# Performance work log

Measured on AMD Instinct MI355X. Metric: run time of the kernel, lower is better.

The kernel has to match this reference:

```python
import jax, jax.numpy as jnp
import numpy as np

B, D, H, Z, E = 65536, 128, 256, 128, 16  # batch, input, hidden, hyper, embedding


def setup_inputs() -> dict:
    key = jax.random.key(0)
    ks = jax.random.split(key, 20)
    s = 0.02  # small weight scale for numerical sanity
    return {
        "x": jax.random.normal(ks[0], (B, D), jnp.float32),
        "h0": jax.random.normal(ks[1], (B, H), jnp.float32),
        "c0": jax.random.normal(ks[2], (B, H), jnp.float32),
        "hhat0": jax.random.normal(ks[3], (B, Z), jnp.float32),
        "chat0": jax.random.normal(ks[4], (B, Z), jnp.float32),
        "hweight": jax.random.normal(ks[5], (Z + H + D, 4 * Z), jnp.float32) * s,
        "hbias": jnp.zeros((4 * Z,), jnp.float32),
        "zw_h": jax.random.normal(ks[6], (Z, 4 * E), jnp.float32) * s,
        "zw_x": jax.random.normal(ks[7], (Z, 4 * E), jnp.float32) * s,
        "zw_b": jax.random.normal(ks[8], (Z, 4 * E), jnp.float32) * 0.01,
        "zb_h": jnp.ones((4 * E,), jnp.float32),
        "zb_x": jnp.ones((4 * E,), jnp.float32),
        "dw_h": jnp.full((4, E, H), 0.1 / E, jnp.float32),  # [i,g,f,o] stacked
        "dw_x": jnp.full((4, E, H), 0.1 / E, jnp.float32),
        "dw_b": jax.random.normal(ks[9], (4, E, H), jnp.float32) * s,
        "weight": jax.random.normal(ks[10], (H + D, 4 * H), jnp.float32) * s,
        "bias": jnp.zeros((4 * H,), jnp.float32),
    }


def reference(x, h0, c0, hhat0, chat0, hweight, hbias, zw_h, zw_x, zw_b,
              zb_h, zb_x, dw_h, dw_x, dw_b, weight, bias):
    sig, tanh = jax.nn.sigmoid, jnp.tanh
    b = x.shape[0]
    # hyper LSTM cell
    gh = jnp.concatenate([hhat0, h0, x], axis=1) @ hweight + hbias  # [B, 4Z]
    i_h, g_h, f_h, o_h = jnp.split(gh, 4, axis=1)
    chat1 = sig(f_h) * chat0 + sig(i_h) * tanh(g_h)
    hhat1 = sig(o_h) * tanh(chat1)
    # embedding projections z (chunk order i,g,f,o -> reshape to [B,4,E])
    z_h = (hhat1 @ zw_h + zb_h).reshape(b, 4, E)
    z_x = (hhat1 @ zw_x + zb_x).reshape(b, 4, E)
    z_b = (hhat1 @ zw_b).reshape(b, 4, E)
    # d scaling vectors, [B,4,H] -> [B,4H]
    d_yh = jnp.einsum('bke,keh->bkh', z_h, dw_h).reshape(b, 4 * H)
    d_yx = jnp.einsum('bke,keh->bkh', z_x, dw_x).reshape(b, 4 * H)
    d_yb = jnp.einsum('bke,keh->bkh', z_b, dw_b).reshape(b, 4 * H)
    # main LSTM gates, hyper-modulated
    g = jnp.concatenate([h0, x], axis=1) @ weight * d_yh * d_yx + d_yb + bias
    i_g, g_g, f_g, o_g = jnp.split(g, 4, axis=1)
    c1 = sig(f_g) * c0 + sig(i_g) * tanh(g_g)
    h1 = sig(o_g) * tanh(c1)
    return (h1, c1, hhat1, chat1)
```

## Files before the change

### kernel.cpp

```cpp
#include <hip/hip_runtime.h>


typedef unsigned short u16;
typedef __attribute__((ext_vector_type(8))) short bf16x8;
typedef __attribute__((ext_vector_type(4))) float f32x4;

#define BATCH 65536

__device__ __forceinline__ u16 f2b(float f) {
  unsigned u = __float_as_uint(f);
  u += 0x7fffu + ((u >> 16) & 1u);
  return (u16)(u >> 16);
}
__device__ __forceinline__ unsigned pk2(float a, float b) {
  return (unsigned)f2b(a) | ((unsigned)f2b(b) << 16);
}
__device__ __forceinline__ float upk_lo(unsigned u) { return __uint_as_float(u << 16); }
__device__ __forceinline__ float upk_hi(unsigned u) { return __uint_as_float(u & 0xffff0000u); }
__device__ __forceinline__ float sigf(float x) { return 1.0f / (1.0f + __expf(-x)); }
__device__ __forceinline__ float tanhfast(float x) {
  float xc = fminf(fmaxf(x, -15.f), 15.f);
  float e = __expf(2.f * xc);
  return (e - 1.f) / (e + 1.f);
}
__device__ __forceinline__ int swz(int r, int c) { return r * 64 + (c ^ ((r & 7) << 3)); }

__device__ __forceinline__ void wait0_bar() {
  asm volatile("s_waitcnt vmcnt(0)" ::: "memory");
  __builtin_amdgcn_s_barrier();
  __builtin_amdgcn_sched_barrier(0);
}

__device__ __forceinline__ void gl_lds16(const u16* g, u16* l) {
  __builtin_amdgcn_global_load_lds(
      (const __attribute__((address_space(1))) void*)g,
      (__attribute__((address_space(3))) void*)l, 16, 0, 0);
}
__device__ __forceinline__ void stageA(const u16* base, int ldk, u16* lA, int t) {
  const int r = t >> 3, q = t & 7, wid = t >> 6;
  const int qs = (q ^ (r & 7)) << 3;
  gl_lds16(base + (size_t)r * ldk + qs, lA + wid * 512);
  gl_lds16(base + (size_t)(r + 32) * ldk + qs, lA + 2048 + wid * 512);
}
__device__ __forceinline__ void stageB16(const u16* tile, u16* lB, int t) {
  const int wid = t >> 6;
#pragma unroll
  for (int i = 0; i < 4; ++i)
    gl_lds16(tile + ((size_t)i * 256 + t) * 8, lB + i * 2048 + wid * 512);
}

__global__ __launch_bounds__(256) void hlstm_pre(
    const float* __restrict__ hhat0, const float* __restrict__ h0,
    const float* __restrict__ x, u16* __restrict__ abuf,
    const float* __restrict__ hweight, const float* __restrict__ hbias,
    const float* __restrict__ zw_h, const float* __restrict__ zw_x, const float* __restrict__ zw_b,
    const float* __restrict__ zb_h, const float* __restrict__ zb_x,
    const float* __restrict__ dw_h, const float* __restrict__ dw_x, const float* __restrict__ dw_b,
    const float* __restrict__ weight, const float* __restrict__ bias,
    u16* __restrict__ hw_fr, float* __restrict__ hbias_r,
    u16* __restrict__ w_fr,  float* __restrict__ bias_r,
    u16* __restrict__ whp_fr, u16* __restrict__ wxp_fr, u16* __restrict__ wbp_fr,
    float* __restrict__ bhp_r, float* __restrict__ bxp_r)
{
  if (blockIdx.x < 4096) {
    const size_t stride = (size_t)4096 * 256;
    for (size_t i = (size_t)blockIdx.x * 256 + threadIdx.x;
         i < (size_t)BATCH * 64; i += stride) {
      const size_t b = i >> 6; const int c = (int)(i & 63);
      const float* src;
      if (c < 16)      src = hhat0 + b * 128 + c * 8;
      else if (c < 48) src = h0 + b * 256 + (size_t)(c - 16) * 8;
      else             src = x + b * 128 + (size_t)(c - 48) * 8;
      float4 v0 = ((const float4*)src)[0];
      float4 v1 = ((const float4*)src)[1];
      alignas(16) u16 o[8] = {f2b(v0.x), f2b(v0.y), f2b(v0.z), f2b(v0.w),
                              f2b(v1.x), f2b(v1.y), f2b(v1.z), f2b(v1.w)};
      *(uint4*)(abuf + i * 8) = *(const uint4*)o;
    }
    return;
  }
  const int tid = (blockIdx.x - 4096) * 256 + threadIdx.x;
  const int nt  = 512 * 256;

  for (int i = tid; i < 32 * 8192; i += nt) {
    int tile = i >> 13, r = i & 8191;
    int wn = r >> 12, h = (r >> 11) & 1, g = (r >> 9) & 3;
    int lane = (r >> 3) & 63, j = r & 7;
    int hb = tile >> 4, hh32 = (tile >> 3) & 1, s = tile & 7;
    int k = s * 64 + h * 32 + (lane >> 4) * 8 + j;
    int col = g * 128 + hb * 64 + hh32 * 32 + wn * 16 + (lane & 15);
    hw_fr[i] = f2b(hweight[k * 512 + col]);
  }
  for (int i = tid; i < 48 * 8192; i += nt) {
    int tile = i >> 13, r = i & 8191;
    int wn = r >> 12, h = (r >> 11) & 1, g = (r >> 9) & 3;
    int lane = (r >> 3) & 63, j = r & 7;
    int hb = tile / 12, rem = tile % 12;
    int hh32 = rem / 6, s = rem % 6;
    int k = s * 64 + h * 32 + (lane >> 4) * 8 + j;
    int col = g * 256 + hb * 64 + hh32 * 32 + wn * 16 + (lane & 15);
    w_fr[i] = f2b(weight[k * 1024 + col]);
  }
  for (int i = tid; i < 3 * 16 * 8192; i += nt) {
    int mat = i / 131072, rem2 = i % 131072;
    int tile = rem2 >> 13, r = rem2 & 8191;
    int wn = r >> 12, h = (r >> 11) & 1, g = (r >> 9) & 3;
    int lane = (r >> 3) & 63, j = r & 7;
    int hb = tile >> 2, hh32 = (tile >> 1) & 1, s = tile & 1;
    int k = s * 64 + h * 32 + (lane >> 4) * 8 + j;
    int colh = hb * 64 + hh32 * 32 + wn * 16 + (lane & 15);
    const float* zw = (mat == 0) ? zw_h : (mat == 1) ? zw_x : zw_b;
    const float* dw = (mat == 0) ? dw_h : (mat == 1) ? dw_x : dw_b;
    float sv = 0.f;
#pragma unroll
    for (int e = 0; e < 16; ++e)
      sv += zw[k * 64 + g * 16 + e] * dw[g * 4096 + e * 256 + colh];
    u16* dst = (mat == 0) ? whp_fr : (mat == 1) ? wxp_fr : wbp_fr;
    dst[rem2] = f2b(sv);
  }
  for (int i = tid; i < 1024; i += nt) {
    int hb = i >> 8, g = (i >> 6) & 3, hh = i & 63;
    int h = hb * 64 + hh;
    float sh = 0.f, sx = 0.f;
#pragma unroll
    for (int e = 0; e < 16; ++e) {
      sh += zb_h[g * 16 + e] * dw_h[g * 4096 + e * 256 + h];
      sx += zb_x[g * 16 + e] * dw_x[g * 4096 + e * 256 + h];
    }
    bhp_r[i] = sh; bxp_r[i] = sx;
    bias_r[i] = bias[g * 256 + h];
  }
  for (int i = tid; i < 512; i += nt) {
    int gate = (i >> 6) & 3, hb = i >> 8, hh = i & 63;
    hbias_r[i] = hbias[gate * 128 + hb * 64 + hh];
  }
}

__global__ __launch_bounds__(256, 2) void hlstm_k1(
    const u16* __restrict__ abuf, const float* __restrict__ chat0,
    const u16* __restrict__ hw_fr, const float* __restrict__ hbias_r,
    float* __restrict__ d_out, u16* __restrict__ hbuf)
{
  __shared__ alignas(16) u16 lA[2][8192];
  __shared__ alignas(16) u16 lB[2][8192];
  const int f = blockIdx.x;
  const int xcd = f & 7, u = f >> 3;
  const int rb = xcd * 64 + (u >> 2);
  const int sub = u & 3, hb = sub >> 1, hh32 = sub & 1;
  const int t = threadIdx.x;
  const int lane = t & 63, w = t >> 6;
  const int wm = w >> 1, wn = w & 1;
  const int lr = lane & 15, kg = lane >> 4;

  f32x4 acc[4][4];
  const f32x4 zzero = {0.f, 0.f, 0.f, 0.f};
#pragma unroll
  for (int mf = 0; mf < 4; ++mf)
#pragma unroll
    for (int g = 0; g < 4; ++g) acc[mf][g] = zzero;

  const u16* arow = abuf + (size_t)rb * 128 * 512;
  auto btile = [&](int s) -> const u16* {
    return hw_fr + (size_t)((hb * 2 + hh32) * 8 + s) * 8192;
  };
  auto stage = [&](int s, int buf) {
    stageA(arow + s * 64, 512, lA[buf], t);
    stageA(arow + s * 64 + (size_t)64 * 512, 512, lA[buf] + 4096, t);
    stageB16(btile(s), lB[buf], t);
  };
  auto sweep = [&](const u16* cA, const u16* cB) {
#pragma unroll
    for (int h = 0; h < 2; ++h) {
      bf16x8 bfr[4];
#pragma unroll
      for (int g = 0; g < 4; ++g)
        bfr[g] = *(const bf16x8*)&cB[wn * 4096 + (h * 4 + g) * 512 + lane * 8];
#pragma unroll
      for (int mf = 0; mf < 4; ++mf) {
        bf16x8 afr = *(const bf16x8*)&cA[swz(wm * 64 + mf * 16 + lr, h * 32 + kg * 8)];
#pragma unroll
        for (int g = 0; g < 4; ++g)
          acc[mf][g] = __builtin_amdgcn_mfma_f32_16x16x32_bf16(afr, bfr[g], acc[mf][g], 0, 0, 0);
      }
    }
  };

  stage(0, 0);
  wait0_bar();
#pragma unroll
  for (int ks = 0; ks < 8; ++ks) {
    const int cur = ks & 1;
    if (ks < 7) stage(ks + 1, cur ^ 1);
    sweep(lA[cur], lB[cur]);
    if (ks < 7) wait0_bar();
  }

  float hb4[4];
#pragma unroll
  for (int g = 0; g < 4; ++g)
    hb4[g] = hbias_r[hb * 256 + g * 64 + hh32 * 32 + wn * 16 + lr];
  const int zc = hb * 64 + hh32 * 32 + wn * 16 + lr;
  float* out_hh = d_out + (size_t)BATCH * 512;
  float* out_ch = d_out + (size_t)BATCH * 640;
#pragma unroll
  for (int mf = 0; mf < 4; ++mf)
#pragma unroll
    for (int r = 0; r < 4; ++r) {
      const int row = rb * 128 + wm * 64 + mf * 16 + kg * 4 + r;
      const float gi = acc[mf][0][r] + hb4[0];
      const float gg = acc[mf][1][r] + hb4[1];
      const float gf = acc[mf][2][r] + hb4[2];
      const float go = acc[mf][3][r] + hb4[3];
      const float c0v = chat0[(size_t)row * 128 + zc];
      const float c1v = sigf(gf) * c0v + sigf(gi) * tanhfast(gg);
      const float h1v = sigf(go) * tanhfast(c1v);
      out_hh[(size_t)row * 128 + zc] = h1v;
      out_ch[(size_t)row * 128 + zc] = c1v;
      hbuf[(size_t)row * 128 + zc] = f2b(h1v);
    }
}

__global__ __launch_bounds__(256, 2) void hlstm_k2(
    const u16* __restrict__ abuf, const u16* __restrict__ hbuf,
    const float* __restrict__ c0,
    const u16* __restrict__ w_fr, const float* __restrict__ bias_r,
    const u16* __restrict__ whp_fr, const u16* __restrict__ wxp_fr, const u16* __restrict__ wbp_fr,
    const float* __restrict__ bhp_r, const float* __restrict__ bxp_r,
    float* __restrict__ d_out)
{
  __shared__ alignas(16) u16 lA[2][8192];
  __shared__ alignas(16) u16 lB[2][8192];
  const int f = blockIdx.x;
  const int xcd = f & 7, u = f >> 3;
  const int rb = xcd * 64 + (u >> 3);
  const int sub = u & 7, hb = sub >> 1, hh32 = sub & 1;
  const int t = threadIdx.x;
  const int lane = t & 63, w = t >> 6;
  const int wm = w >> 1, wn = w & 1;
  const int lr = lane & 15, kg = lane >> 4;

  const u16* amain = abuf + (size_t)rb * 128 * 512 + 128;
  const u16* ahyp  = hbuf + (size_t)rb * 128 * 128;

  auto aptr = [&](int s) -> const u16* {
    if (s >= 4 && s < 10) return amain + (s - 4) * 64;
    return ahyp + (s & 1) * 64;
  };
  auto aldk = [&](int s) -> int { return (s >= 4 && s < 10) ? 512 : 128; };
  auto bptr = [&](int s) -> const u16* {
    const int base = (hb * 2 + hh32);
    if (s < 2)  return whp_fr + (size_t)(base * 2 + s) * 8192;
    if (s < 4)  return wxp_fr + (size_t)(base * 2 + s - 2) * 8192;
    if (s < 10) return w_fr  + (size_t)(base * 6 + s - 4) * 8192;
    return wbp_fr + (size_t)(base * 2 + s - 10) * 8192;
  };

  f32x4 acc[4][4];
  const f32x4 zzero = {0.f, 0.f, 0.f, 0.f};
#pragma unroll
  for (int mf = 0; mf < 4; ++mf)
#pragma unroll
    for (int g = 0; g < 4; ++g) acc[mf][g] = zzero;

  unsigned dsc[4][4][2];

  auto stage = [&](int s, int buf) {
    const u16* ap = aptr(s); const int ldk = aldk(s);
    stageA(ap, ldk, lA[buf], t);
    stageA(ap + (size_t)64 * ldk, ldk, lA[buf] + 4096, t);
    stageB16(bptr(s), lB[buf], t);
  };
  auto sweep = [&](const u16* cA, const u16* cB) {
#pragma unroll
    for (int h = 0; h < 2; ++h) {
      bf16x8 bfr[4];
#pragma unroll
      for (int g = 0; g < 4; ++g)
        bfr[g] = *(const bf16x8*)&cB[wn * 4096 + (h * 4 + g) * 512 + lane * 8];
#pragma unroll
      for (int mf = 0; mf < 4; ++mf) {
        bf16x8 afr = *(const bf16x8*)&cA[swz(wm * 64 + mf * 16 + lr, h * 32 + kg * 8)];
#pragma unroll
        for (int g = 0; g < 4; ++g)
          acc[mf][g] = __builtin_amdgcn_mfma_f32_16x16x32_bf16(afr, bfr[g], acc[mf][g], 0, 0, 0);
      }
    }
  };

  stage(0, 0);
  wait0_bar();
#pragma unroll
  for (int s = 0; s < 12; ++s) {
    const int cur = s & 1;
    if (s < 11) stage(s + 1, cur ^ 1);
    if (s == 2 || s == 4) {
#pragma unroll
      for (int mf = 0; mf < 4; ++mf)
#pragma unroll
        for (int g = 0; g < 4; ++g) acc[mf][g] = zzero;
    }
    sweep(lA[cur], lB[cur]);

    if (s == 1) {
      float bh4[4];
#pragma unroll
      for (int g = 0; g < 4; ++g)
        bh4[g] = bhp_r[hb * 256 + g * 64 + hh32 * 32 + wn * 16 + lr];
#pragma unroll
      for (int mf = 0; mf < 4; ++mf)
#pragma unroll
        for (int g = 0; g < 4; ++g) {
          dsc[mf][g][0] = pk2(acc[mf][g][0] + bh4[g], acc[mf][g][1] + bh4[g]);
          dsc[mf][g][1] = pk2(acc[mf][g][2] + bh4[g], acc[mf][g][3] + bh4[g]);
        }
    } else if (s == 3) {
      float bx4[4];
#pragma unroll
      for (int g = 0; g < 4; ++g)
        bx4[g] = bxp_r[hb * 256 + g * 64 + hh32 * 32 + wn * 16 + lr];
#pragma unroll
      for (int mf = 0; mf < 4; ++mf)
#pragma unroll
        for (int g = 0; g < 4; ++g) {
          float d0 = upk_lo(dsc[mf][g][0]) * (acc[mf][g][0] + bx4[g]);
          float d1 = upk_hi(dsc[mf][g][0]) * (acc[mf][g][1] + bx4[g]);
          float d2 = upk_lo(dsc[mf][g][1]) * (acc[mf][g][2] + bx4[g]);
          float d3 = upk_hi(dsc[mf][g][1]) * (acc[mf][g][3] + bx4[g]);
          dsc[mf][g][0] = pk2(d0, d1);
          dsc[mf][g][1] = pk2(d2, d3);
        }
    } else if (s == 9) {
#pragma unroll
      for (int mf = 0; mf < 4; ++mf)
#pragma unroll
        for (int g = 0; g < 4; ++g) {
          acc[mf][g][0] *= upk_lo(dsc[mf][g][0]);
          acc[mf][g][1] *= upk_hi(dsc[mf][g][0]);
          acc[mf][g][2] *= upk_lo(dsc[mf][g][1]);
          acc[mf][g][3] *= upk_hi(dsc[mf][g][1]);
        }
    }
    if (s < 11) wait0_bar();
  }

  const int hcol = hb * 64 + hh32 * 32 + wn * 16 + lr;
  float b4[4];
#pragma unroll
  for (int g = 0; g < 4; ++g)
    b4[g] = bias_r[hb * 256 + g * 64 + hh32 * 32 + wn * 16 + lr];
  float* out_c1 = d_out + (size_t)BATCH * 256;
#pragma unroll
  for (int mf = 0; mf < 4; ++mf)
#pragma unroll
    for (int r = 0; r < 4; ++r) {
      const int row = rb * 128 + wm * 64 + mf * 16 + kg * 4 + r;
      const float gi = acc[mf][0][r] + b4[0];
      const float gg = acc[mf][1][r] + b4[1];
      const float gf = acc[mf][2][r] + b4[2];
      const float go = acc[mf][3][r] + b4[3];
      const float c0v = c0[(size_t)row * 256 + hcol];
      const float c1v = sigf(gf) * c0v + sigf(gi) * tanhfast(gg);
      const float h1v = sigf(go) * tanhfast(c1v);
      d_out[(size_t)row * 256 + hcol]  = h1v;
      out_c1[(size_t)row * 256 + hcol] = c1v;
    }
}

extern "C" void kernel_launch(void* const* d_in, const int* in_sizes, int n_in,
                              void* d_out, int out_size, void* d_ws, size_t ws_size,
                              hipStream_t stream)
{
  (void)in_sizes; (void)n_in; (void)out_size; (void)ws_size;
  const float* x       = (const float*)d_in[0];
  const float* h0      = (const float*)d_in[1];
  const float* c0      = (const float*)d_in[2];
  const float* hhat0   = (const float*)d_in[3];
  const float* chat0   = (const float*)d_in[4];
  const float* hweight = (const float*)d_in[5];
  const float* hbias   = (const float*)d_in[6];
  const float* zw_h    = (const float*)d_in[7];
  const float* zw_x    = (const float*)d_in[8];
  const float* zw_b    = (const float*)d_in[9];
  const float* zb_h    = (const float*)d_in[10];
  const float* zb_x    = (const float*)d_in[11];
  const float* dw_h    = (const float*)d_in[12];
  const float* dw_x    = (const float*)d_in[13];
  const float* dw_b    = (const float*)d_in[14];
  const float* weight  = (const float*)d_in[15];
  const float* bias    = (const float*)d_in[16];

  char* wsb = (char*)d_ws;
  u16*   abuf    = (u16*)(wsb + 0);
  u16*   hbuf    = (u16*)(wsb + 67108864);
  u16*   hw_fr   = (u16*)(wsb + 83886080);
  u16*   w_fr    = (u16*)(wsb + 84410368);
  u16*   whp_fr  = (u16*)(wsb + 85196800);
  u16*   wxp_fr  = (u16*)(wsb + 85458944);
  u16*   wbp_fr  = (u16*)(wsb + 85721088);
  float* hbias_r = (float*)(wsb + 85983232);
  float* bias_r  = (float*)(wsb + 85985280);
  float* bhp_r   = (float*)(wsb + 85989376);
  float* bxp_r   = (float*)(wsb + 85993472);

  hlstm_pre<<<dim3(4608), dim3(256), 0, stream>>>(
      hhat0, h0, x, abuf,
      hweight, hbias, zw_h, zw_x, zw_b, zb_h, zb_x, dw_h, dw_x, dw_b, weight, bias,
      hw_fr, hbias_r, w_fr, bias_r, whp_fr, wxp_fr, wbp_fr, bhp_r, bxp_r);

  hlstm_k1<<<dim3(2048), dim3(256), 0, stream>>>(
      abuf, chat0, hw_fr, hbias_r, (float*)d_out, hbuf);

  hlstm_k2<<<dim3(4096), dim3(256), 0, stream>>>(
      abuf, hbuf, c0, w_fr, bias_r, whp_fr, wxp_fr, wbp_fr, bhp_r, bxp_r, (float*)d_out);
}
```

Before: 278.5 us.

## Use 512-thread blocks with 256-row tiles and triple-buffered LDS pipeline

Both GEMM kernels now use 512 threads (8 waves) per block covering 256 rows instead of 128, so each B tile staged in LDS is reused across twice as many rows. The LDS pipeline goes from double to triple buffering: loads are issued two stages ahead, and a partial vmcnt wait replaces the full drain before each barrier. MFMA sweeps are wrapped in s_setprio to favour the math waves. The cost is larger LDS use per block (about 144KB), which limits residency to one block per CU.

```diff
diff --git a/kernel.cpp b/kernel.cpp
--- a/kernel.cpp
+++ b/kernel.cpp
@@ -25,28 +25,25 @@
 }
 __device__ __forceinline__ int swz(int r, int c) { return r * 64 + (c ^ ((r & 7) << 3)); }
 
-__device__ __forceinline__ void wait0_bar() {
-  asm volatile("s_waitcnt vmcnt(0)" ::: "memory");
-  __builtin_amdgcn_s_barrier();
-  __builtin_amdgcn_sched_barrier(0);
-}
+#define VM_BAR(N) do { \
+  asm volatile("s_waitcnt vmcnt(" #N ")" ::: "memory"); \
+  __builtin_amdgcn_s_barrier(); \
+  __builtin_amdgcn_sched_barrier(0); } while (0)
 
 __device__ __forceinline__ void gl_lds16(const u16* g, u16* l) {
   __builtin_amdgcn_global_load_lds(
       (const __attribute__((address_space(1))) void*)g,
       (__attribute__((address_space(3))) void*)l, 16, 0, 0);
 }
-__device__ __forceinline__ void stageA(const u16* base, int ldk, u16* lA, int t) {
-  const int r = t >> 3, q = t & 7, wid = t >> 6;
-  const int qs = (q ^ (r & 7)) << 3;
-  gl_lds16(base + (size_t)r * ldk + qs, lA + wid * 512);
-  gl_lds16(base + (size_t)(r + 32) * ldk + qs, lA + 2048 + wid * 512);
-}
-__device__ __forceinline__ void stageB16(const u16* tile, u16* lB, int t) {
-  const int wid = t >> 6;
-#pragma unroll
-  for (int i = 0; i < 4; ++i)
-    gl_lds16(tile + ((size_t)i * 256 + t) * 8, lB + i * 2048 + wid * 512);
+__device__ __forceinline__ void stageA512(const u16* base, int ldk, u16* sub, int t) {
+  const int r = t >> 3, q = t & 7;
+  gl_lds16(base + (size_t)r * ldk + (((q ^ (r & 7)) << 3)), sub + (t >> 6) * 512);
+}
+__device__ __forceinline__ void stageB512(const u16* tile, u16* lB, int t) {
+  const int w = t >> 6;
+#pragma unroll
+  for (int i = 0; i < 2; ++i)
+    gl_lds16(tile + ((size_t)i * 512 + t) * 8, lB + i * 4096 + w * 512);
 }
 
 __global__ __launch_bounds__(256) void hlstm_pre(
@@ -136,16 +133,16 @@
   }
 }
 
-__global__ __launch_bounds__(256, 2) void hlstm_k1(
+__global__ __launch_bounds__(512) void hlstm_k1(
     const u16* __restrict__ abuf, const float* __restrict__ chat0,
     const u16* __restrict__ hw_fr, const float* __restrict__ hbias_r,
     float* __restrict__ d_out, u16* __restrict__ hbuf)
 {
-  __shared__ alignas(16) u16 lA[2][8192];
-  __shared__ alignas(16) u16 lB[2][8192];
+  __shared__ alignas(16) u16 lA[3][16384];
+  __shared__ alignas(16) u16 lB[3][8192];
   const int f = blockIdx.x;
   const int xcd = f & 7, u = f >> 3;
-  const int rb = xcd * 64 + (u >> 2);
+  const int rb = xcd * 32 + (u >> 2);
   const int sub = u & 3, hb = sub >> 1, hh32 = sub & 1;
   const int t = threadIdx.x;
   const int lane = t & 63, w = t >> 6;
@@ -159,16 +156,15 @@
 #pragma unroll
     for (int g = 0; g < 4; ++g) acc[mf][g] = zzero;
 
-  const u16* arow = abuf + (size_t)rb * 128 * 512;
-  auto btile = [&](int s) -> const u16* {
-    return hw_fr + (size_t)((hb * 2 + hh32) * 8 + s) * 8192;
-  };
+  const u16* arow = abuf + (size_t)rb * 256 * 512;
   auto stage = [&](int s, int buf) {
-    stageA(arow + s * 64, 512, lA[buf], t);
-    stageA(arow + s * 64 + (size_t)64 * 512, 512, lA[buf] + 4096, t);
-    stageB16(btile(s), lB[buf], t);
+#pragma unroll
+    for (int m = 0; m < 4; ++m)
+      stageA512(arow + (size_t)(m * 64) * 512 + s * 64, 512, lA[buf] + m * 4096, t);
+    stageB512(hw_fr + (size_t)((hb * 2 + hh32) * 8 + s) * 8192, lB[buf], t);
   };
   auto sweep = [&](const u16* cA, const u16* cB) {
+    __builtin_amdgcn_s_setprio(1);
 #pragma unroll
     for (int h = 0; h < 2; ++h) {
       bf16x8 bfr[4];
@@ -177,22 +173,23 @@
         bfr[g] = *(const bf16x8*)&cB[wn * 4096 + (h * 4 + g) * 512 + lane * 8];
 #pragma unroll
       for (int mf = 0; mf < 4; ++mf) {
-        bf16x8 afr = *(const bf16x8*)&cA[swz(wm * 64 + mf * 16 + lr, h * 32 + kg * 8)];
+        bf16x8 afr = *(const bf16x8*)&cA[wm * 4096 + swz(mf * 16 + lr, h * 32 + kg * 8)];
 #pragma unroll
         for (int g = 0; g < 4; ++g)
           acc[mf][g] = __builtin_amdgcn_mfma_f32_16x16x32_bf16(afr, bfr[g], acc[mf][g], 0, 0, 0);
       }
     }
+    __builtin_amdgcn_s_setprio(0);
   };
 
   stage(0, 0);
-  wait0_bar();
+  stage(1, 1);
 #pragma unroll
   for (int ks = 0; ks < 8; ++ks) {
-    const int cur = ks & 1;
-    if (ks < 7) stage(ks + 1, cur ^ 1);
-    sweep(lA[cur], lB[cur]);
-    if (ks < 7) wait0_bar();
+    if (ks < 7) VM_BAR(6);
+    else        VM_BAR(0);
+    if (ks < 6) stage(ks + 2, (ks + 2) % 3);
+    sweep(lA[ks % 3], lB[ks % 3]);
   }
 
   float hb4[4];
@@ -206,7 +203,7 @@
   for (int mf = 0; mf < 4; ++mf)
 #pragma unroll
     for (int r = 0; r < 4; ++r) {
-      const int row = rb * 128 + wm * 64 + mf * 16 + kg * 4 + r;
+      const int row = rb * 256 + wm * 64 + mf * 16 + kg * 4 + r;
       const float gi = acc[mf][0][r] + hb4[0];
       const float gg = acc[mf][1][r] + hb4[1];
       const float gf = acc[mf][2][r] + hb4[2];
@@ -220,7 +217,7 @@
     }
 }
 
-__global__ __launch_bounds__(256, 2) void hlstm_k2(
+__global__ __launch_bounds__(512) void hlstm_k2(
     const u16* __restrict__ abuf, const u16* __restrict__ hbuf,
     const float* __restrict__ c0,
     const u16* __restrict__ w_fr, const float* __restrict__ bias_r,
@@ -228,19 +225,19 @@
     const float* __restrict__ bhp_r, const float* __restrict__ bxp_r,
     float* __restrict__ d_out)
 {
-  __shared__ alignas(16) u16 lA[2][8192];
-  __shared__ alignas(16) u16 lB[2][8192];
+  __shared__ alignas(16) u16 lA[3][16384];
+  __shared__ alignas(16) u16 lB[3][8192];
   const int f = blockIdx.x;
   const int xcd = f & 7, u = f >> 3;
-  const int rb = xcd * 64 + (u >> 3);
+  const int rb = xcd * 32 + (u >> 3);
   const int sub = u & 7, hb = sub >> 1, hh32 = sub & 1;
   const int t = threadIdx.x;
   const int lane = t & 63, w = t >> 6;
   const int wm = w >> 1, wn = w & 1;
   const int lr = lane & 15, kg = lane >> 4;
 
-  const u16* amain = abuf + (size_t)rb * 128 * 512 + 128;
-  const u16* ahyp  = hbuf + (size_t)rb * 128 * 128;
+  const u16* amain = abuf + (size_t)rb * 256 * 512 + 128;
+  const u16* ahyp  = hbuf + (size_t)rb * 256 * 128;
 
   auto aptr = [&](int s) -> const u16* {
     if (s >= 4 && s < 10) return amain + (s - 4) * 64;
@@ -266,11 +263,13 @@
 
   auto stage = [&](int s, int buf) {
     const u16* ap = aptr(s); const int ldk = aldk(s);
-    stageA(ap, ldk, lA[buf], t);
-    stageA(ap + (size_t)64 * ldk, ldk, lA[buf] + 4096, t);
-    stageB16(bptr(s), lB[buf], t);
+#pragma unroll
+    for (int m = 0; m < 4; ++m)
+      stageA512(ap + (size_t)(m * 64) * ldk, ldk, lA[buf] + m * 4096, t);
+    stageB512(bptr(s), lB[buf], t);
   };
   auto sweep = [&](const u16* cA, const u16* cB) {
+    __builtin_amdgcn_s_setprio(1);
 #pragma unroll
     for (int h = 0; h < 2; ++h) {
       bf16x8 bfr[4];
@@ -279,27 +278,29 @@
         bfr[g] = *(const bf16x8*)&cB[wn * 4096 + (h * 4 + g) * 512 + lane * 8];
 #pragma unroll
       for (int mf = 0; mf < 4; ++mf) {
-        bf16x8 afr = *(const bf16x8*)&cA[swz(wm * 64 + mf * 16 + lr, h * 32 + kg * 8)];
+        bf16x8 afr = *(const bf16x8*)&cA[wm * 4096 + swz(mf * 16 + lr, h * 32 + kg * 8)];
 #pragma unroll
         for (int g = 0; g < 4; ++g)
           acc[mf][g] = __builtin_amdgcn_mfma_f32_16x16x32_bf16(afr, bfr[g], acc[mf][g], 0, 0, 0);
       }
     }
+    __builtin_amdgcn_s_setprio(0);
   };
 
   stage(0, 0);
-  wait0_bar();
+  stage(1, 1);
 #pragma unroll
   for (int s = 0; s < 12; ++s) {
-    const int cur = s & 1;
-    if (s < 11) stage(s + 1, cur ^ 1);
+    if (s < 11) VM_BAR(6);
+    else        VM_BAR(0);
+    if (s < 10) stage(s + 2, (s + 2) % 3);
     if (s == 2 || s == 4) {
 #pragma unroll
       for (int mf = 0; mf < 4; ++mf)
 #pragma unroll
         for (int g = 0; g < 4; ++g) acc[mf][g] = zzero;
     }
-    sweep(lA[cur], lB[cur]);
+    sweep(lA[s % 3], lB[s % 3]);
 
     if (s == 1) {
       float bh4[4];
@@ -340,7 +341,6 @@
           acc[mf][g][3] *= upk_hi(dsc[mf][g][1]);
         }
     }
-    if (s < 11) wait0_bar();
   }
 
   const int hcol = hb * 64 + hh32 * 32 + wn * 16 + lr;
@@ -353,7 +353,7 @@
   for (int mf = 0; mf < 4; ++mf)
 #pragma unroll
     for (int r = 0; r < 4; ++r) {
-      const int row = rb * 128 + wm * 64 + mf * 16 + kg * 4 + r;
+      const int row = rb * 256 + wm * 64 + mf * 16 + kg * 4 + r;
       const float gi = acc[mf][0][r] + b4[0];
       const float gg = acc[mf][1][r] + b4[1];
       const float gf = acc[mf][2][r] + b4[2];
@@ -407,9 +407,9 @@
       hweight, hbias, zw_h, zw_x, zw_b, zb_h, zb_x, dw_h, dw_x, dw_b, weight, bias,
       hw_fr, hbias_r, w_fr, bias_r, whp_fr, wxp_fr, wbp_fr, bhp_r, bxp_r);
 
-  hlstm_k1<<<dim3(2048), dim3(256), 0, stream>>>(
+  hlstm_k1<<<dim3(1024), dim3(512), 0, stream>>>(
       abuf, chat0, hw_fr, hbias_r, (float*)d_out, hbuf);
 
-  hlstm_k2<<<dim3(4096), dim3(256), 0, stream>>>(
+  hlstm_k2<<<dim3(2048), dim3(512), 0, stream>>>(
       abuf, hbuf, c0, w_fr, bias_r, whp_fr, wxp_fr, wbp_fr, bhp_r, bxp_r, (float*)d_out);
 }
```

After: 293.2 us. 1.05x slower.
